# Performance work log

Hardware: AMD Instinct MI355X
Metric: run time of the kernel (lower is better)

Reference implementation:

```python
import jax, jax.numpy as jnp
import numpy as np

VOCAB = 50257
EMB = 512
HID = 1024
H = HID // 2  # per-direction hidden
TAGS = 24
START = 22
STOP = 23
SEQ = 4096
NEG = -10000.0


def setup_inputs() -> dict:
    key = jax.random.key(0)
    ks = jax.random.split(key, 16)
    s = 1.0 / np.sqrt(H)
    u = lambda k, shp: jax.random.uniform(k, shp, jnp.float32, -s, s)
    sentence = jax.random.randint(ks[0], (SEQ,), 0, VOCAB)
    emb = jax.random.normal(ks[1], (VOCAB, EMB), jnp.float32)
    w_ih_f = u(ks[2], (4 * H, EMB)); w_hh_f = u(ks[3], (4 * H, H))
    b_ih_f = u(ks[4], (4 * H,));    b_hh_f = u(ks[5], (4 * H,))
    w_ih_b = u(ks[6], (4 * H, EMB)); w_hh_b = u(ks[7], (4 * H, H))
    b_ih_b = u(ks[8], (4 * H,));    b_hh_b = u(ks[9], (4 * H,))
    w_tag = u(ks[10], (TAGS, HID)); b_tag = u(ks[11], (TAGS,))
    transitions = jax.random.normal(ks[12], (TAGS, TAGS), jnp.float32)
    transitions = transitions.at[START, :].set(NEG).at[:, STOP].set(NEG)
    h0 = jax.random.normal(ks[13], (2, H), jnp.float32)  # [dir, H]
    c0 = jax.random.normal(ks[14], (2, H), jnp.float32)
    return dict(sentence=sentence, emb=emb,
                w_ih_f=w_ih_f, w_hh_f=w_hh_f, b_ih_f=b_ih_f, b_hh_f=b_hh_f,
                w_ih_b=w_ih_b, w_hh_b=w_hh_b, b_ih_b=b_ih_b, b_hh_b=b_hh_b,
                w_tag=w_tag, b_tag=b_tag, transitions=transitions, h0=h0, c0=c0)


def _lstm_dir(x, w_ih, w_hh, b_ih, b_hh, h, c, reverse):
    # x: [T, EMB]; precompute input projections once
    xg = x @ w_ih.T + (b_ih + b_hh)  # [T, 4H]
    def step(carry, xt):
        h, c = carry
        g = xt + h @ w_hh.T
        i, f, gg, o = jnp.split(g, 4)
        i = jax.nn.sigmoid(i); f = jax.nn.sigmoid(f)
        gg = jnp.tanh(gg);     o = jax.nn.sigmoid(o)
        c = f * c + i * gg
        h = o * jnp.tanh(c)
        return (h, c), h
    _, hs = jax.lax.scan(step, (h, c), xg, reverse=reverse)
    return hs  # [T, H]


def reference(sentence, emb, w_ih_f, w_hh_f, b_ih_f, b_hh_f,
              w_ih_b, w_hh_b, b_ih_b, b_hh_b, w_tag, b_tag,
              transitions, h0, c0):
    x = emb[sentence]  # [T, EMB]
    hf = _lstm_dir(x, w_ih_f, w_hh_f, b_ih_f, b_hh_f, h0[0], c0[0], False)
    hb = _lstm_dir(x, w_ih_b, w_hh_b, b_ih_b, b_hh_b, h0[1], c0[1], True)
    lstm_out = jnp.concatenate([hf, hb], axis=-1)          # [T, HID]
    feats = lstm_out @ w_tag.T + b_tag                     # [T, TAGS]

    # Viterbi: max-plus recursion over tags, vectorized per timestep
    fv0 = jnp.full((TAGS,), NEG, jnp.float32).at[START].set(0.0)
    def vstep(fv, feat):
        scores = transitions + fv[None, :]                 # [next, prev]
        bp = jnp.argmax(scores, axis=1)
        return jnp.max(scores, axis=1) + feat, bp
    fv, bps = jax.lax.scan(vstep, fv0, feats)              # bps: [T, TAGS]

    terminal = fv + transitions[STOP]
    best = jnp.argmax(terminal)
    path_score = terminal[best]

    def btstep(tag, bp):
        prev = bp[tag]
        return prev, prev
    _, ys = jax.lax.scan(btstep, best, bps, reverse=True)  # ys[t] = tag at t-1; ys[0]==START
    best_path = jnp.concatenate([ys[1:], best[None]]).astype(jnp.int32)
    return path_score, best_path
```

## Files before the change

### kernel.cpp

```cpp
#include <hip/hip_runtime.h>
#include <cstdint>
#include <cstddef>

#define T_SEQ 4096
#define EMB_D 512
#define HDIM 512
#define G4 2048
#define NTAGS 24
#define START_TAG 22
#define STOP_TAG 23
#define NEGV -10000.0f
#define NBLK 32
#define HSLICE 16
#define SENT 0xFFFFFFFFu

__global__ __launch_bounds__(256) void gemm_xg_kernel(
    const int* __restrict__ sent, const float* __restrict__ emb,
    const float* __restrict__ w_ih_f, const float* __restrict__ b_ih_f, const float* __restrict__ b_hh_f,
    const float* __restrict__ w_ih_b, const float* __restrict__ b_ih_b, const float* __restrict__ b_hh_b,
    float* __restrict__ xg)
{
    const int dir = blockIdx.z;
    const float* W  = dir ? w_ih_b : w_ih_f;
    const float* bi = dir ? b_ih_b : b_ih_f;
    const float* bh = dir ? b_hh_b : b_hh_f;
    const int m0 = blockIdx.y * 64;
    const int n0 = blockIdx.x * 64;
    const int tid = threadIdx.x;

    __shared__ __attribute__((aligned(16))) float As[32][64];
    __shared__ __attribute__((aligned(16))) float Bs[32][64];

    const int lrow = tid >> 2;
    const int lk   = (tid & 3) * 8;

    const int srow = sent[m0 + lrow];
    const float* aptr = emb + (size_t)srow * EMB_D + lk;
    const float* bptr = W   + (size_t)(n0 + lrow) * EMB_D + lk;

    const int ty = tid >> 4;
    const int tx = tid & 15;

    float acc[4][4];
    #pragma unroll
    for (int i = 0; i < 4; ++i)
        #pragma unroll
        for (int j = 0; j < 4; ++j) acc[i][j] = 0.f;

    for (int kk = 0; kk < EMB_D; kk += 32) {
        float4 a0 = *(const float4*)(aptr + kk);
        float4 a1 = *(const float4*)(aptr + kk + 4);
        float4 b0 = *(const float4*)(bptr + kk);
        float4 b1 = *(const float4*)(bptr + kk + 4);
        __syncthreads();
        As[lk+0][lrow]=a0.x; As[lk+1][lrow]=a0.y; As[lk+2][lrow]=a0.z; As[lk+3][lrow]=a0.w;
        As[lk+4][lrow]=a1.x; As[lk+5][lrow]=a1.y; As[lk+6][lrow]=a1.z; As[lk+7][lrow]=a1.w;
        Bs[lk+0][lrow]=b0.x; Bs[lk+1][lrow]=b0.y; Bs[lk+2][lrow]=b0.z; Bs[lk+3][lrow]=b0.w;
        Bs[lk+4][lrow]=b1.x; Bs[lk+5][lrow]=b1.y; Bs[lk+6][lrow]=b1.z; Bs[lk+7][lrow]=b1.w;
        __syncthreads();
        #pragma unroll
        for (int k = 0; k < 32; ++k) {
            float4 av = *(const float4*)&As[k][ty*4];
            float4 bv = *(const float4*)&Bs[k][tx*4];
            acc[0][0]+=av.x*bv.x; acc[0][1]+=av.x*bv.y; acc[0][2]+=av.x*bv.z; acc[0][3]+=av.x*bv.w;
            acc[1][0]+=av.y*bv.x; acc[1][1]+=av.y*bv.y; acc[1][2]+=av.y*bv.z; acc[1][3]+=av.y*bv.w;
            acc[2][0]+=av.z*bv.x; acc[2][1]+=av.z*bv.y; acc[2][2]+=av.z*bv.z; acc[2][3]+=av.z*bv.w;
            acc[3][0]+=av.w*bv.x; acc[3][1]+=av.w*bv.y; acc[3][2]+=av.w*bv.z; acc[3][3]+=av.w*bv.w;
        }
    }
    #pragma unroll
    for (int i = 0; i < 4; ++i) {
        const int t = m0 + ty*4 + i;
        float* crow = xg + ((size_t)dir*T_SEQ + t) * G4 + n0 + tx*4;
        #pragma unroll
        for (int j = 0; j < 4; ++j) {
            const int jg = n0 + tx*4 + j;
            crow[j] = acc[i][j] + bi[jg] + bh[jg];
        }
    }
}

__global__ __launch_bounds__(512, 1) void bilstm_kernel(
    const float* __restrict__ w_hh_f, const float* __restrict__ w_hh_b,
    const float* __restrict__ h0, const float* __restrict__ c0,
    const float* __restrict__ xg,
    uint32_t* __restrict__ h_hist)
{
    const int blk = blockIdx.x;
    const int dir = blk >> 5;
    const int b   = blk & 31;
    const int tid = threadIdx.x;
    const int q   = tid >> 6;
    const int rl  = tid & 63;
    const int g2  = rl >> 4;
    const int hu  = rl & 15;
    const int row = g2 * HDIM + b * HSLICE + hu;

    const float* Wrow = (dir ? w_hh_b : w_hh_f) + (size_t)row * HDIM + q * 64;
    float4 w4[16];
    #pragma unroll
    for (int j = 0; j < 16; ++j) w4[j] = ((const float4*)Wrow)[j];

    __shared__ __attribute__((aligned(16))) float hbuf[512];
    __shared__ float part[512];

    float c = (tid < HSLICE) ? c0[dir*HDIM + b*HSLICE + tid] : 0.f;

    const float* xgd = xg + (size_t)dir * T_SEQ * G4;
    uint32_t* hh = h_hist + (size_t)dir * T_SEQ * HDIM;

    for (int idx = 0; idx < T_SEQ; ++idx) {
        const int t = dir ? (T_SEQ - 1 - idx) : idx;
        float xv = 0.f;
        if (tid < 64) xv = xgd[(size_t)t * G4 + row];

        if (idx == 0) {
            hbuf[tid] = h0[dir*HDIM + tid];
        } else {
            const int tprev = dir ? (t + 1) : (t - 1);
            const uint32_t* wp = hh + (size_t)tprev*HDIM + tid;
            uint32_t u;
            do {
                u = __hip_atomic_load(wp, __ATOMIC_RELAXED, __HIP_MEMORY_SCOPE_AGENT);
            } while (u == SENT);
            union { uint32_t u; float f; } cv; cv.u = u;
            hbuf[tid] = cv.f;
        }
        __syncthreads();

        float s = 0.f;
        const float4* hb4 = (const float4*)&hbuf[q*64];
        #pragma unroll
        for (int j = 0; j < 16; ++j) {
            float4 hv = hb4[j];
            s += w4[j].x*hv.x + w4[j].y*hv.y + w4[j].z*hv.z + w4[j].w*hv.w;
        }
        part[tid] = s;
        __syncthreads();

        if (tid < 64) {
            float g = xv;
            #pragma unroll
            for (int qq = 0; qq < 8; ++qq) g += part[qq*64 + tid];
            g = (g2 == 2) ? tanhf(g) : 1.f/(1.f + expf(-g));
            float iv = __shfl(g, hu);
            float fg = __shfl(g, hu + 16);
            float gv = __shfl(g, hu + 32);
            float ov = __shfl(g, hu + 48);
            if (tid < HSLICE) {
                c = fg*c + iv*gv;
                union { float f; uint32_t u; } hb; hb.f = ov * tanhf(c);
                __hip_atomic_store(hh + (size_t)t*HDIM + b*HSLICE + tid, hb.u,
                                   __ATOMIC_RELAXED, __HIP_MEMORY_SCOPE_AGENT);
            }
        }
    }
}

__global__ __launch_bounds__(256) void feats_kernel(
    const float* __restrict__ h_hist, const float* __restrict__ w_tag,
    const float* __restrict__ b_tag, float* __restrict__ feats)
{
    const int t = blockIdx.x;
    const int tid = threadIdx.x;
    __shared__ __attribute__((aligned(16))) float h[1024];
    __shared__ float partl[192];
    for (int i = tid; i < 512; i += 256) {
        h[i]     = h_hist[(size_t)t*HDIM + i];
        h[512+i] = h_hist[(size_t)T_SEQ*HDIM + (size_t)t*HDIM + i];
    }
    __syncthreads();
    if (tid < 192) {
        const int tag = tid >> 3, p = tid & 7;
        const float* wr = w_tag + (size_t)tag*1024 + p*128;
        const float* hp = h + p*128;
        float s = 0.f;
        #pragma unroll 8
        for (int j = 0; j < 128; ++j) s += wr[j]*hp[j];
        partl[tid] = s;
    }
    __syncthreads();
    if (tid < NTAGS) {
        float s = b_tag[tid];
        #pragma unroll
        for (int p = 0; p < 8; ++p) s += partl[tid*8+p];
        feats[(size_t)t*NTAGS + tid] = s;
    }
}

__global__ void viterbi_fwd_kernel(
    const float* __restrict__ feats, const float* __restrict__ trans,
    float* __restrict__ d_out, unsigned char* __restrict__ bp,
    int* __restrict__ best_tag)
{
    const int lane = threadIdx.x;
    const bool act = lane < NTAGS;
    float tr[NTAGS];
    #pragma unroll
    for (int p = 0; p < NTAGS; ++p)
        tr[p] = act ? trans[lane*NTAGS + p] : NEGV;

    float fv = (lane == START_TAG) ? 0.f : NEGV;
    __shared__ float fvs[NTAGS];
    __shared__ float term[NTAGS];

    float ftn = act ? feats[lane] : 0.f;
    for (int t = 0; t < T_SEQ; ++t) {
        if (act) fvs[lane] = fv;
        __syncthreads();
        float ft = ftn;
        if (act && t + 1 < T_SEQ) ftn = feats[(size_t)(t+1)*NTAGS + lane];
        float bestv = -3.4e38f;
        int argp = 0;
        #pragma unroll
        for (int p = 0; p < NTAGS; ++p) {
            float sc = tr[p] + fvs[p];
            if (sc > bestv) { bestv = sc; argp = p; }
        }
        __syncthreads();
        fv = bestv + ft;
        if (act) bp[(size_t)t*NTAGS + lane] = (unsigned char)argp;
    }
    if (act) { fv += trans[STOP_TAG*NTAGS + lane]; term[lane] = fv; }
    __syncthreads();
    if (lane == 0) {
        float bv = term[0]; int bi = 0;
        #pragma unroll
        for (int p = 1; p < NTAGS; ++p) if (term[p] > bv) { bv = term[p]; bi = p; }
        d_out[0] = bv;
        *best_tag = bi;
    }
}

__global__ void bt_compose_kernel(const unsigned char* __restrict__ bp,
                                  unsigned char* __restrict__ segmap)
{
    const int s = blockIdx.x;
    const int tid = threadIdx.x;
    __shared__ __attribute__((aligned(16))) unsigned char lbp[64*NTAGS];
    const uint32_t* src = (const uint32_t*)(bp + (size_t)s * 64 * NTAGS);
    uint32_t* dst = (uint32_t*)lbp;
    #pragma unroll
    for (int i = 0; i < 6; ++i) dst[tid + 64*i] = src[tid + 64*i];
    __syncthreads();
    if (tid < NTAGS) {
        int m = tid;
        for (int tt = 63; tt >= 0; --tt) m = lbp[tt*NTAGS + m];
        segmap[s*NTAGS + tid] = (unsigned char)m;
    }
}

__global__ void bt_final_kernel(const unsigned char* __restrict__ segmap,
                                const int* __restrict__ best_tag,
                                int* __restrict__ end_tags)
{
    if (threadIdx.x == 0) {
        int tag = *best_tag;
        end_tags[63] = tag;
        for (int s = 63; s >= 1; --s) {
            tag = segmap[s*NTAGS + tag];
            end_tags[s-1] = tag;
        }
    }
}

__global__ void bt_write_kernel(const unsigned char* __restrict__ bp,
                                const int* __restrict__ end_tags,
                                float* __restrict__ out_path)
{
    const int s = blockIdx.x;
    const int tid = threadIdx.x;
    __shared__ __attribute__((aligned(16))) unsigned char lbp[64*NTAGS];
    const uint32_t* src = (const uint32_t*)(bp + (size_t)s * 64 * NTAGS);
    uint32_t* dst = (uint32_t*)lbp;
    #pragma unroll
    for (int i = 0; i < 6; ++i) dst[tid + 64*i] = src[tid + 64*i];
    __syncthreads();
    if (tid == 0) {
        int tag = end_tags[s];
        out_path[s*64 + 63] = (float)tag;
        for (int tt = 63; tt >= 1; --tt) {
            tag = lbp[tt*NTAGS + tag];
            out_path[s*64 + tt - 1] = (float)tag;
        }
    }
}

extern "C" void kernel_launch(void* const* d_in, const int* in_sizes, int n_in,
                              void* d_out, int out_size, void* d_ws, size_t ws_size,
                              hipStream_t stream)
{
    const int*   sent   = (const int*)d_in[0];
    const float* emb    = (const float*)d_in[1];
    const float* w_ih_f = (const float*)d_in[2];
    const float* w_hh_f = (const float*)d_in[3];
    const float* b_ih_f = (const float*)d_in[4];
    const float* b_hh_f = (const float*)d_in[5];
    const float* w_ih_b = (const float*)d_in[6];
    const float* w_hh_b = (const float*)d_in[7];
    const float* b_ih_b = (const float*)d_in[8];
    const float* b_hh_b = (const float*)d_in[9];
    const float* w_tag  = (const float*)d_in[10];
    const float* b_tag  = (const float*)d_in[11];
    const float* trans  = (const float*)d_in[12];
    const float* h0     = (const float*)d_in[13];
    const float* c0     = (const float*)d_in[14];
    float* out = (float*)d_out;

    char* ws = (char*)d_ws;
    size_t off = 0;
    auto alloc = [&](size_t bytes) {
        char* p = ws + off; off += (bytes + 255) & ~(size_t)255; return p;
    };
    float* xg      = (float*)alloc((size_t)2*T_SEQ*G4*sizeof(float));
    uint32_t* h_hist = (uint32_t*)alloc((size_t)2*T_SEQ*HDIM*sizeof(float));
    float* feats   = (float*)alloc((size_t)T_SEQ*NTAGS*sizeof(float));
    unsigned char* bp     = (unsigned char*)alloc((size_t)T_SEQ*NTAGS);
    unsigned char* segmap = (unsigned char*)alloc(64*NTAGS);
    int* best_tag = (int*)alloc(sizeof(int));
    int* end_tags = (int*)alloc(64*sizeof(int));

    if (off > ws_size) {
        hipMemsetAsync(d_out, 0xFF, 4, stream);
        return;
    }

    hipMemsetAsync(h_hist, 0xFF, (size_t)2*T_SEQ*HDIM*sizeof(float), stream);

    dim3 gg(G4/64, T_SEQ/64, 2);
    gemm_xg_kernel<<<gg, 256, 0, stream>>>(sent, emb,
        w_ih_f, b_ih_f, b_hh_f, w_ih_b, b_ih_b, b_hh_b, xg);
    bilstm_kernel<<<64, 512, 0, stream>>>(w_hh_f, w_hh_b, h0, c0, xg, h_hist);
    feats_kernel<<<T_SEQ, 256, 0, stream>>>((const float*)h_hist, w_tag, b_tag, feats);
    viterbi_fwd_kernel<<<1, 64, 0, stream>>>(feats, trans, out, bp, best_tag);
    bt_compose_kernel<<<64, 64, 0, stream>>>(bp, segmap);
    bt_final_kernel<<<1, 64, 0, stream>>>(segmap, best_tag, end_tags);
    bt_write_kernel<<<64, 64, 0, stream>>>(bp, end_tags, out + 1);
}
```

Before: 9.453 ms.

## Make each wave own two hidden units to remove block barriers in LSTM step

The recurrent step is restructured so each 64-lane wavefront computes all four gates for two hidden units, with weights held in registers and the dot product reduced by cross-lane shuffles. This drops the shared-memory staging of h and both __syncthreads per timestep. In exchange every wave now polls all 512 h values from global memory on its own, and each gate needs a 6-step shuffle reduction, so there are many more shuffles per step.

```diff
diff --git a/kernel.cpp b/kernel.cpp
--- a/kernel.cpp
+++ b/kernel.cpp
@@ -90,69 +90,86 @@
     const int dir = blk >> 5;
     const int b   = blk & 31;
     const int tid = threadIdx.x;
-    const int q   = tid >> 6;
+    const int wv  = tid >> 6;
     const int rl  = tid & 63;
-    const int g2  = rl >> 4;
-    const int hu  = rl & 15;
-    const int row = g2 * HDIM + b * HSLICE + hu;
-
-    const float* Wrow = (dir ? w_hh_b : w_hh_f) + (size_t)row * HDIM + q * 64;
-    float4 w4[16];
-    #pragma unroll
-    for (int j = 0; j < 16; ++j) w4[j] = ((const float4*)Wrow)[j];
-
-    __shared__ __attribute__((aligned(16))) float hbuf[512];
-    __shared__ float part[512];
-
-    float c = (tid < HSLICE) ? c0[dir*HDIM + b*HSLICE + tid] : 0.f;
+
+    const int u0 = b * HSLICE + 2 * wv;
+    const float* W = dir ? w_hh_b : w_hh_f;
+
+    float wreg[8][8];
+    #pragma unroll
+    for (int j = 0; j < 8; ++j) {
+        const float* wp = W + (size_t)((j >> 1) * HDIM + u0 + (j & 1)) * HDIM + rl;
+        #pragma unroll
+        for (int k = 0; k < 8; ++k) wreg[j][k] = wp[64 * k];
+    }
+    #pragma unroll
+    for (int j = 0; j < 8; ++j)
+        #pragma unroll
+        for (int k = 0; k < 8; ++k)
+            asm volatile("" : "+v"(wreg[j][k]));
+
+    float cA = c0[dir * HDIM + u0];
+    float cB = c0[dir * HDIM + u0 + 1];
 
     const float* xgd = xg + (size_t)dir * T_SEQ * G4;
     uint32_t* hh = h_hist + (size_t)dir * T_SEQ * HDIM;
+    const int myrow = (rl >> 1) * HDIM + u0 + (rl & 1);
 
     for (int idx = 0; idx < T_SEQ; ++idx) {
         const int t = dir ? (T_SEQ - 1 - idx) : idx;
-        float xv = 0.f;
-        if (tid < 64) xv = xgd[(size_t)t * G4 + row];
-
+        float xgv = 0.f;
+        if (rl < 8) xgv = xgd[(size_t)t * G4 + myrow];
+
+        float h8[8];
         if (idx == 0) {
-            hbuf[tid] = h0[dir*HDIM + tid];
+            #pragma unroll
+            for (int k = 0; k < 8; ++k) h8[k] = h0[dir * HDIM + rl + 64 * k];
         } else {
             const int tprev = dir ? (t + 1) : (t - 1);
-            const uint32_t* wp = hh + (size_t)tprev*HDIM + tid;
-            uint32_t u;
-            do {
-                u = __hip_atomic_load(wp, __ATOMIC_RELAXED, __HIP_MEMORY_SCOPE_AGENT);
-            } while (u == SENT);
-            union { uint32_t u; float f; } cv; cv.u = u;
-            hbuf[tid] = cv.f;
-        }
-        __syncthreads();
-
-        float s = 0.f;
-        const float4* hb4 = (const float4*)&hbuf[q*64];
-        #pragma unroll
-        for (int j = 0; j < 16; ++j) {
-            float4 hv = hb4[j];
-            s += w4[j].x*hv.x + w4[j].y*hv.y + w4[j].z*hv.z + w4[j].w*hv.w;
-        }
-        part[tid] = s;
-        __syncthreads();
-
-        if (tid < 64) {
-            float g = xv;
-            #pragma unroll
-            for (int qq = 0; qq < 8; ++qq) g += part[qq*64 + tid];
-            g = (g2 == 2) ? tanhf(g) : 1.f/(1.f + expf(-g));
-            float iv = __shfl(g, hu);
-            float fg = __shfl(g, hu + 16);
-            float gv = __shfl(g, hu + 32);
-            float ov = __shfl(g, hu + 48);
-            if (tid < HSLICE) {
-                c = fg*c + iv*gv;
-                union { float f; uint32_t u; } hb; hb.f = ov * tanhf(c);
-                __hip_atomic_store(hh + (size_t)t*HDIM + b*HSLICE + tid, hb.u,
-                                   __ATOMIC_RELAXED, __HIP_MEMORY_SCOPE_AGENT);
+            const uint32_t* pp = hh + (size_t)tprev * HDIM + rl;
+            uint32_t u[8];
+            #pragma unroll
+            for (int k = 0; k < 8; ++k)
+                u[k] = __hip_atomic_load(pp + 64 * k, __ATOMIC_RELAXED,
+                                         __HIP_MEMORY_SCOPE_AGENT);
+            #pragma unroll
+            for (int k = 0; k < 8; ++k)
+                while (u[k] == SENT)
+                    u[k] = __hip_atomic_load(pp + 64 * k, __ATOMIC_RELAXED,
+                                             __HIP_MEMORY_SCOPE_AGENT);
+            #pragma unroll
+            for (int k = 0; k < 8; ++k) {
+                union { uint32_t u; float f; } cv; cv.u = u[k]; h8[k] = cv.f;
             }
+        }
+
+        float g[8];
+        #pragma unroll
+        for (int j = 0; j < 8; ++j) {
+            float s = 0.f;
+            #pragma unroll
+            for (int k = 0; k < 8; ++k) s += wreg[j][k] * h8[k];
+            #pragma unroll
+            for (int m = 1; m < 64; m <<= 1) s += __shfl_xor(s, m, 64);
+            g[j] = s + __shfl(xgv, j, 64);
+        }
+        float a0 = 1.f/(1.f + expf(-g[0]));
+        float a1 = 1.f/(1.f + expf(-g[1]));
+        float a2 = 1.f/(1.f + expf(-g[2]));
+        float a3 = 1.f/(1.f + expf(-g[3]));
+        float a4 = tanhf(g[4]);
+        float a5 = tanhf(g[5]);
+        float a6 = 1.f/(1.f + expf(-g[6]));
+        float a7 = 1.f/(1.f + expf(-g[7]));
+        cA = a2 * cA + a0 * a4;
+        cB = a3 * cB + a1 * a5;
+        float hA = a6 * tanhf(cA);
+        float hB = a7 * tanhf(cB);
+        if (rl < 2) {
+            union { float f; uint32_t u; } hb; hb.f = rl ? hB : hA;
+            __hip_atomic_store(hh + (size_t)t * HDIM + u0 + rl, hb.u,
+                               __ATOMIC_RELAXED, __HIP_MEMORY_SCOPE_AGENT);
         }
     }
 }
```

Result: slower. 24.88 ms (+163.2%).
